# Kernel optimization log

Hardware: AMD Instinct MI355X
Metric: run time of the kernel (lower is better)

The kernel has to match this reference:

```python
import jax, jax.numpy as jnp
import numpy as np

B, H, W = 8, 256, 256
CP = 1            # pattern channels
CIN = CP + 2      # total state channels
K = 3             # neighborhood size
HID = 256         # hidden dim
ALPHA = 0.5
T_STEPS = 128
IN_DIM = CIN * K * K  # 27


def _patches(x):
    # Equivalent of tf.image.extract_patches with SAME zero padding.
    # x: [B,H,W,C] -> [B,H,W,K*K*C], ordered (kh, kw, c) with c fastest,
    # matching TF's patch flattening.
    p = (K - 1) // 2
    xp = jnp.pad(x, ((0, 0), (p, p), (p, p), (0, 0)))
    shifts = [xp[:, i:i + H, j:j + W, :] for i in range(K) for j in range(K)]
    return jnp.concatenate(shifts, axis=-1)


def setup_inputs() -> dict:
    key = jax.random.key(0)
    ks = jax.random.split(key, 5)
    state = jax.random.uniform(ks[0], (B, H, W, CIN), dtype=jnp.float32)
    # Dense layer params (glorot-ish scaling)
    W1 = jax.random.normal(ks[1], (IN_DIM, HID), dtype=jnp.float32) / np.sqrt(IN_DIM)
    b1 = jnp.zeros((HID,), dtype=jnp.float32)
    W2 = jax.random.normal(ks[2], (HID, CP), dtype=jnp.float32) / np.sqrt(HID)
    b2 = jnp.zeros((CP,), dtype=jnp.float32)
    return {"state": state, "W1": W1, "b1": b1, "W2": W2, "b2": b2}


def reference(state, W1, b1, W2, b2):
    def step(s, _):
        flat = _patches(s)                       # [B,H,W,27]
        h = jnp.tanh(flat @ W1 + b1)             # [B,H,W,HID]
        delta = h @ W2 + b2                      # [B,H,W,CP]
        pat = jnp.clip(s[..., :CP] + ALPHA * delta, 0.0, 1.0)
        s = jnp.concatenate([pat, s[..., CP:]], axis=-1)
        return s, None

    out, _ = jax.lax.scan(step, state, None, length=T_STEPS)
    return out
```

## Files before the change

kernel.cpp:

```cpp
#include <hip/hip_runtime.h>


#define BATCH 8
#define HGT 256
#define WID 256
#define NHID 256
#define ALPHA 0.5f

#define WS_W1T_OFF (BATCH * HGT * WID * 3)
#define WS_W2_OFF  (WS_W1T_OFF + 28 * NHID)

__device__ __forceinline__ float tanh_xla(float x) {
    const float cl = 7.90531110763549805f;
    float xc = fminf(fmaxf(x, -cl), cl);
    float x2 = xc * xc;
    float p = fmaf(x2, -2.76076847742355e-16f, 2.00018790482477e-13f);
    p = fmaf(x2, p, -8.60467152213735e-11f);
    p = fmaf(x2, p, 5.12229709037114e-08f);
    p = fmaf(x2, p, 1.48572235717979e-05f);
    p = fmaf(x2, p, 6.37261928875436e-04f);
    p = fmaf(x2, p, 4.89352455891786e-03f);
    p = xc * p;
    float q = fmaf(x2, 1.19825839466702e-06f, 1.18534705686654e-04f);
    q = fmaf(x2, q, 2.26843463243900e-03f);
    q = fmaf(x2, q, 4.89352518554385e-03f);
    float r = p / q;
    return (fabsf(x) < 0.0004f) ? x : r;
}

__global__ __launch_bounds__(256) void nca_prep(const float* __restrict__ W1,
                                                const float* __restrict__ b1,
                                                const float* __restrict__ W2,
                                                float* __restrict__ ws) {
    int n = threadIdx.x;
    float* w1t = ws + WS_W1T_OFF;
#pragma unroll
    for (int k = 0; k < 27; ++k) w1t[n * 28 + k] = W1[k * NHID + n];
    w1t[n * 28 + 27] = b1[n];
    ws[WS_W2_OFF + n] = W2[n];
}

#define MM1_CHAIN(P, ACC)                                   \
    do {                                                    \
        ACC = fmaf(X[0][0 + P][0], w0.x, ACC);              \
        ACC = fmaf(X[0][0 + P][1], w0.y, ACC);              \
        ACC = fmaf(X[0][0 + P][2], w0.z, ACC);              \
        ACC = fmaf(X[0][1 + P][0], w0.w, ACC);              \
        ACC = fmaf(X[0][1 + P][1], w1.x, ACC);              \
        ACC = fmaf(X[0][1 + P][2], w1.y, ACC);              \
        ACC = fmaf(X[0][2 + P][0], w1.z, ACC);              \
        ACC = fmaf(X[0][2 + P][1], w1.w, ACC);              \
        ACC = fmaf(X[0][2 + P][2], w2v.x, ACC);             \
        ACC = fmaf(X[1][0 + P][0], w2v.y, ACC);             \
        ACC = fmaf(X[1][0 + P][1], w2v.z, ACC);             \
        ACC = fmaf(X[1][0 + P][2], w2v.w, ACC);             \
        ACC = fmaf(X[1][1 + P][0], w3.x, ACC);              \
        ACC = fmaf(X[1][1 + P][1], w3.y, ACC);              \
        ACC = fmaf(X[1][1 + P][2], w3.z, ACC);              \
        ACC = fmaf(X[1][2 + P][0], w3.w, ACC);              \
        ACC = fmaf(X[1][2 + P][1], w4.x, ACC);              \
        ACC = fmaf(X[1][2 + P][2], w4.y, ACC);              \
        ACC = fmaf(X[2][0 + P][0], w4.z, ACC);              \
        ACC = fmaf(X[2][0 + P][1], w4.w, ACC);              \
        ACC = fmaf(X[2][0 + P][2], w5.x, ACC);              \
        ACC = fmaf(X[2][1 + P][0], w5.y, ACC);              \
        ACC = fmaf(X[2][1 + P][1], w5.z, ACC);              \
        ACC = fmaf(X[2][1 + P][2], w5.w, ACC);              \
        ACC = fmaf(X[2][2 + P][0], w6.x, ACC);              \
        ACC = fmaf(X[2][2 + P][1], w6.y, ACC);              \
        ACC = fmaf(X[2][2 + P][2], w6.z, ACC);              \
        ACC = ACC + w6.w;                      \
    } while (0)

__global__ __launch_bounds__(256)
__attribute__((amdgpu_waves_per_eu(2, 2)))
void nca_step(const float* __restrict__ sin,
              float* __restrict__ sout,
              const float* __restrict__ w1t,
              const float* __restrict__ w2,
              const float* __restrict__ b2p) {
    const int gid = blockIdx.x * 256 + threadIdx.x;
    const int xq = gid & 63;
    const int y  = (gid >> 6) & 255;
    const int b  = gid >> 14;
    const int x0 = xq * 4;

    float X[3][6][3];
#pragma unroll
    for (int r = 0; r < 3; ++r) {
        const int yy = y + r - 1;
        const bool yok = (yy >= 0) && (yy < HGT);
        const float* rowp = sin + (((long)b * HGT + (yok ? yy : 0)) * WID) * 3;
#pragma unroll
        for (int cc = 0; cc < 6; ++cc) {
            const int xx = x0 + cc - 1;
            const bool ok = yok && (xx >= 0) && (xx < WID);
            if (ok) {
                X[r][cc][0] = rowp[xx * 3 + 0];
                X[r][cc][1] = rowp[xx * 3 + 1];
                X[r][cc][2] = rowp[xx * 3 + 2];
            } else {
                X[r][cc][0] = 0.f; X[r][cc][1] = 0.f; X[r][cc][2] = 0.f;
            }
        }
    }
#pragma unroll
    for (int r = 0; r < 3; ++r)
#pragma unroll
        for (int cc = 0; cc < 6; ++cc)
#pragma unroll
            for (int c = 0; c < 3; ++c)
                asm volatile("" : "+v"(X[r][cc][c]));

    const float4* __restrict__ wq = (const float4*)w1t;

    float delta0 = 0.f, delta1 = 0.f, delta2 = 0.f, delta3 = 0.f;

    for (int n = 0; n < NHID; ++n) {
        const float4 w0  = wq[n * 7 + 0];
        const float4 w1  = wq[n * 7 + 1];
        const float4 w2v = wq[n * 7 + 2];
        const float4 w3  = wq[n * 7 + 3];
        const float4 w4  = wq[n * 7 + 4];
        const float4 w5  = wq[n * 7 + 5];
        const float4 w6  = wq[n * 7 + 6];
        const float  w2n = w2[n];

        float a0 = 0.f, a1 = 0.f, a2 = 0.f, a3 = 0.f;
        MM1_CHAIN(0, a0);
        MM1_CHAIN(1, a1);
        MM1_CHAIN(2, a2);
        MM1_CHAIN(3, a3);
        const float h0 = tanh_xla(a0);
        const float h1 = tanh_xla(a1);
        const float h2 = tanh_xla(a2);
        const float h3 = tanh_xla(a3);
        delta0 = fmaf(h0, w2n, delta0);
        delta1 = fmaf(h1, w2n, delta1);
        delta2 = fmaf(h2, w2n, delta2);
        delta3 = fmaf(h3, w2n, delta3);
    }

    const float b2v = b2p[0];
    float* op = sout + (((long)b * HGT + y) * WID + x0) * 3;
    float dl[4] = {delta0, delta1, delta2, delta3};
#pragma unroll
    for (int p = 0; p < 4; ++p) {
        const float s0 = X[1][p + 1][0];
        const float d  = dl[p] + b2v;
        const float td = ALPHA * d;
        float pat = s0 + td;
        pat = fminf(fmaxf(pat, 0.f), 1.f);
        op[p * 3 + 0] = pat;
        op[p * 3 + 1] = X[1][p + 1][1];
        op[p * 3 + 2] = X[1][p + 1][2];
    }
}

extern "C" void kernel_launch(void* const* d_in, const int* in_sizes, int n_in,
                              void* d_out, int out_size, void* d_ws, size_t ws_size,
                              hipStream_t stream) {
    const float* state = (const float*)d_in[0];
    const float* W1    = (const float*)d_in[1];
    const float* b1    = (const float*)d_in[2];
    const float* W2    = (const float*)d_in[3];
    const float* b2    = (const float*)d_in[4];

    float* ws_state = (float*)d_ws;
    float* w1t      = ws_state + WS_W1T_OFF;
    float* w2c      = ws_state + WS_W2_OFF;
    float* out      = (float*)d_out;

    nca_prep<<<1, 256, 0, stream>>>(W1, b1, W2, ws_state);

    const int nblocks = (BATCH * HGT * (WID / 4)) / 256;

    for (int t = 0; t < 128; ++t) {
        const float* in  = (t == 0) ? state : (((t - 1) & 1) ? out : ws_state);
        float*       dst = (t & 1) ? out : ws_state;
        nca_step<<<nblocks, 256, 0, stream>>>(in, dst, w1t, w2c, b2);
    }
}
```

Before: 19.75 ms.

## Skip MLP for pixels whose pattern neighborhood is unchanged since previous step

The pattern channel is stored as its own planar array and rotated through three buffers. The constant channels are read directly from the input state. Each thread now handles 2 pixels instead of 4, and occupancy is raised from 2 to 4 waves per EU. Each thread compares its 3x3 pattern neighborhood with the previous step's; if it is bitwise identical, the output must also be identical, so the thread copies the current value and skips the 256-wide MLP. The skip only pays off when every lane in a wavefront is at a fixed point, and the extra compare loads plus the smaller per-thread tile add cost when few pixels have settled.

```diff
diff --git a/kernel.cpp b/kernel.cpp
--- a/kernel.cpp
+++ b/kernel.cpp
@@ -5,10 +5,14 @@
 #define HGT 256
 #define WID 256
 #define NHID 256
+#define NPIX (BATCH * HGT * WID)
 #define ALPHA 0.5f
 
-#define WS_W1T_OFF (BATCH * HGT * WID * 3)
-#define WS_W2_OFF  (WS_W1T_OFF + 28 * NHID)
+#define WS_P0  0
+#define WS_P1  NPIX
+#define WS_P2  (2 * NPIX)
+#define WS_W1T (3 * NPIX)
+#define WS_W2  (WS_W1T + 28 * NHID)
 
 __device__ __forceinline__ float tanh_xla(float x) {
     const float cl = 7.90531110763549805f;
@@ -33,11 +37,28 @@
                                                 const float* __restrict__ W2,
                                                 float* __restrict__ ws) {
     int n = threadIdx.x;
-    float* w1t = ws + WS_W1T_OFF;
+    float* w1t = ws + WS_W1T;
 #pragma unroll
     for (int k = 0; k < 27; ++k) w1t[n * 28 + k] = W1[k * NHID + n];
     w1t[n * 28 + 27] = b1[n];
-    ws[WS_W2_OFF + n] = W2[n];
+    ws[WS_W2 + n] = W2[n];
+}
+
+__global__ __launch_bounds__(256) void nca_init(const float* __restrict__ state,
+                                                float* __restrict__ P0) {
+    int i = blockIdx.x * 256 + threadIdx.x;
+    if (i < NPIX) P0[i] = state[i * 3];
+}
+
+__global__ __launch_bounds__(256) void nca_final(const float* __restrict__ P,
+                                                 const float* __restrict__ cstate,
+                                                 float* __restrict__ out) {
+    int i = blockIdx.x * 256 + threadIdx.x;
+    if (i < NPIX) {
+        out[i * 3]     = P[i];
+        out[i * 3 + 1] = cstate[i * 3 + 1];
+        out[i * 3 + 2] = cstate[i * 3 + 2];
+    }
 }
 
 #define MM1_CHAIN(P, ACC)                                   \
@@ -73,48 +94,85 @@
     } while (0)
 
 __global__ __launch_bounds__(256)
-__attribute__((amdgpu_waves_per_eu(2, 2)))
-void nca_step(const float* __restrict__ sin,
-              float* __restrict__ sout,
+__attribute__((amdgpu_waves_per_eu(4, 4)))
+void nca_step(const float* __restrict__ Pprev,
+              const float* __restrict__ Pcur,
+              float* __restrict__ Pnext,
+              const float* __restrict__ cstate,
               const float* __restrict__ w1t,
               const float* __restrict__ w2,
-              const float* __restrict__ b2p) {
+              const float* __restrict__ b2p,
+              int first) {
     const int gid = blockIdx.x * 256 + threadIdx.x;
-    const int xq = gid & 63;
-    const int y  = (gid >> 6) & 255;
-    const int b  = gid >> 14;
-    const int x0 = xq * 4;
-
-    float X[3][6][3];
+    const int xq = gid & 127;
+    const int y  = (gid >> 7) & 255;
+    const int b  = gid >> 15;
+    const int x0 = xq * 2;
+
+    float Pc[3][4];
 #pragma unroll
     for (int r = 0; r < 3; ++r) {
         const int yy = y + r - 1;
         const bool yok = (yy >= 0) && (yy < HGT);
-        const float* rowp = sin + (((long)b * HGT + (yok ? yy : 0)) * WID) * 3;
-#pragma unroll
-        for (int cc = 0; cc < 6; ++cc) {
+        const float* prow = Pcur + ((long)b * HGT + (yok ? yy : 0)) * WID;
+#pragma unroll
+        for (int cc = 0; cc < 4; ++cc) {
             const int xx = x0 + cc - 1;
             const bool ok = yok && (xx >= 0) && (xx < WID);
-            if (ok) {
-                X[r][cc][0] = rowp[xx * 3 + 0];
-                X[r][cc][1] = rowp[xx * 3 + 1];
-                X[r][cc][2] = rowp[xx * 3 + 2];
-            } else {
-                X[r][cc][0] = 0.f; X[r][cc][1] = 0.f; X[r][cc][2] = 0.f;
+            Pc[r][cc] = ok ? prow[xx] : 0.f;
+        }
+    }
+
+    const long base = ((long)b * HGT + y) * WID + x0;
+
+    if (!first) {
+        bool same = true;
+#pragma unroll
+        for (int r = 0; r < 3; ++r) {
+            const int yy = y + r - 1;
+            const bool yok = (yy >= 0) && (yy < HGT);
+            const float* prow = Pprev + ((long)b * HGT + (yok ? yy : 0)) * WID;
+#pragma unroll
+            for (int cc = 0; cc < 4; ++cc) {
+                const int xx = x0 + cc - 1;
+                const bool ok = yok && (xx >= 0) && (xx < WID);
+                const float pv = ok ? prow[xx] : 0.f;
+                same = same && (__float_as_uint(Pc[r][cc]) == __float_as_uint(pv));
             }
         }
+        if (same) {
+            Pnext[base]     = Pc[1][1];
+            Pnext[base + 1] = Pc[1][2];
+            return;
+        }
+    }
+
+    float X[3][4][3];
+#pragma unroll
+    for (int r = 0; r < 3; ++r) {
+        const int yy = y + r - 1;
+        const bool yok = (yy >= 0) && (yy < HGT);
+        const float* crow = cstate + (((long)b * HGT + (yok ? yy : 0)) * WID) * 3;
+#pragma unroll
+        for (int cc = 0; cc < 4; ++cc) {
+            const int xx = x0 + cc - 1;
+            const bool ok = yok && (xx >= 0) && (xx < WID);
+            X[r][cc][0] = Pc[r][cc];
+            X[r][cc][1] = ok ? crow[xx * 3 + 1] : 0.f;
+            X[r][cc][2] = ok ? crow[xx * 3 + 2] : 0.f;
+        }
     }
 #pragma unroll
     for (int r = 0; r < 3; ++r)
 #pragma unroll
-        for (int cc = 0; cc < 6; ++cc)
+        for (int cc = 0; cc < 4; ++cc)
 #pragma unroll
             for (int c = 0; c < 3; ++c)
                 asm volatile("" : "+v"(X[r][cc][c]));
 
     const float4* __restrict__ wq = (const float4*)w1t;
 
-    float delta0 = 0.f, delta1 = 0.f, delta2 = 0.f, delta3 = 0.f;
+    float delta0 = 0.f, delta1 = 0.f;
 
     for (int n = 0; n < NHID; ++n) {
         const float4 w0  = wq[n * 7 + 0];
@@ -126,34 +184,31 @@
         const float4 w6  = wq[n * 7 + 6];
         const float  w2n = w2[n];
 
-        float a0 = 0.f, a1 = 0.f, a2 = 0.f, a3 = 0.f;
+        float a0 = 0.f, a1 = 0.f;
         MM1_CHAIN(0, a0);
         MM1_CHAIN(1, a1);
-        MM1_CHAIN(2, a2);
-        MM1_CHAIN(3, a3);
         const float h0 = tanh_xla(a0);
         const float h1 = tanh_xla(a1);
-        const float h2 = tanh_xla(a2);
-        const float h3 = tanh_xla(a3);
         delta0 = fmaf(h0, w2n, delta0);
         delta1 = fmaf(h1, w2n, delta1);
-        delta2 = fmaf(h2, w2n, delta2);
-        delta3 = fmaf(h3, w2n, delta3);
     }
 
     const float b2v = b2p[0];
-    float* op = sout + (((long)b * HGT + y) * WID + x0) * 3;
-    float dl[4] = {delta0, delta1, delta2, delta3};
-#pragma unroll
-    for (int p = 0; p < 4; ++p) {
-        const float s0 = X[1][p + 1][0];
-        const float d  = dl[p] + b2v;
+    {
+        const float s0 = Pc[1][1];
+        const float d  = delta0 + b2v;
         const float td = ALPHA * d;
         float pat = s0 + td;
         pat = fminf(fmaxf(pat, 0.f), 1.f);
-        op[p * 3 + 0] = pat;
-        op[p * 3 + 1] = X[1][p + 1][1];
-        op[p * 3 + 2] = X[1][p + 1][2];
+        Pnext[base] = pat;
+    }
+    {
+        const float s0 = Pc[1][2];
+        const float d  = delta1 + b2v;
+        const float td = ALPHA * d;
+        float pat = s0 + td;
+        pat = fminf(fmaxf(pat, 0.f), 1.f);
+        Pnext[base + 1] = pat;
     }
 }
 
@@ -166,18 +221,23 @@
     const float* W2    = (const float*)d_in[3];
     const float* b2    = (const float*)d_in[4];
 
-    float* ws_state = (float*)d_ws;
-    float* w1t      = ws_state + WS_W1T_OFF;
-    float* w2c      = ws_state + WS_W2_OFF;
-    float* out      = (float*)d_out;
-
-    nca_prep<<<1, 256, 0, stream>>>(W1, b1, W2, ws_state);
-
-    const int nblocks = (BATCH * HGT * (WID / 4)) / 256;
+    float* ws  = (float*)d_ws;
+    float* P[3] = {ws + WS_P0, ws + WS_P1, ws + WS_P2};
+    float* w1t = ws + WS_W1T;
+    float* w2c = ws + WS_W2;
+    float* out = (float*)d_out;
+
+    nca_prep<<<1, 256, 0, stream>>>(W1, b1, W2, ws);
+    nca_init<<<NPIX / 256, 256, 0, stream>>>(state, P[0]);
+
+    const int nblocks = (NPIX / 2) / 256;
 
     for (int t = 0; t < 128; ++t) {
-        const float* in  = (t == 0) ? state : (((t - 1) & 1) ? out : ws_state);
-        float*       dst = (t & 1) ? out : ws_state;
-        nca_step<<<nblocks, 256, 0, stream>>>(in, dst, w1t, w2c, b2);
-    }
-}
+        float* prv = P[(t + 2) % 3];
+        float* cur = P[t % 3];
+        float* nxt = P[(t + 1) % 3];
+        nca_step<<<nblocks, 256, 0, stream>>>(prv, cur, nxt, state,
+                                              w1t, w2c, b2, (t == 0) ? 1 : 0);
+    }
+    nca_final<<<NPIX / 256, 256, 0, stream>>>(P[128 % 3], state, out);
+}
```

Result: no change. 19.90 ms (+0.8%).

## Process two pixels per thread and force weight loads onto vector path

Applied to the files above, without the earlier changes.

Each thread now computes 2 output pixels instead of 4, doubling the grid and raising the occupancy target from 2 to 4 waves per EU. An opaque zero VGPR offset is added to the weight pointer so the compiler emits per-lane vector loads instead of scalar loads, and the hidden loop is unrolled by 2. The aim is more latency hiding through higher occupancy. The cost is less reuse of each weight load across pixels and more redundant neighbourhood loads per output.

```diff
diff --git a/kernel.cpp b/kernel.cpp
--- a/kernel.cpp
+++ b/kernel.cpp
@@ -73,26 +73,26 @@
     } while (0)
 
 __global__ __launch_bounds__(256)
-__attribute__((amdgpu_waves_per_eu(2, 2)))
+__attribute__((amdgpu_waves_per_eu(4, 4)))
 void nca_step(const float* __restrict__ sin,
               float* __restrict__ sout,
               const float* __restrict__ w1t,
               const float* __restrict__ w2,
               const float* __restrict__ b2p) {
     const int gid = blockIdx.x * 256 + threadIdx.x;
-    const int xq = gid & 63;
-    const int y  = (gid >> 6) & 255;
-    const int b  = gid >> 14;
-    const int x0 = xq * 4;
+    const int xq = gid & 127;
+    const int y  = (gid >> 7) & 255;
+    const int b  = gid >> 15;
+    const int x0 = xq * 2;
 
-    float X[3][6][3];
+    float X[3][4][3];
 #pragma unroll
     for (int r = 0; r < 3; ++r) {
         const int yy = y + r - 1;
         const bool yok = (yy >= 0) && (yy < HGT);
         const float* rowp = sin + (((long)b * HGT + (yok ? yy : 0)) * WID) * 3;
 #pragma unroll
-        for (int cc = 0; cc < 6; ++cc) {
+        for (int cc = 0; cc < 4; ++cc) {
             const int xx = x0 + cc - 1;
             const bool ok = yok && (xx >= 0) && (xx < WID);
             if (ok) {
@@ -107,53 +107,59 @@
 #pragma unroll
     for (int r = 0; r < 3; ++r)
 #pragma unroll
-        for (int cc = 0; cc < 6; ++cc)
+        for (int cc = 0; cc < 4; ++cc)
 #pragma unroll
             for (int c = 0; c < 3; ++c)
                 asm volatile("" : "+v"(X[r][cc][c]));
 
-    const float4* __restrict__ wq = (const float4*)w1t;
+    unsigned vz;
+    asm volatile("v_mov_b32 %0, 0" : "=v"(vz));
+    const float4* __restrict__ wqv =
+        (const float4*)((const char*)w1t + vz);
 
-    float delta0 = 0.f, delta1 = 0.f, delta2 = 0.f, delta3 = 0.f;
+    float delta0 = 0.f, delta1 = 0.f;
 
+#pragma unroll 2
     for (int n = 0; n < NHID; ++n) {
-        const float4 w0  = wq[n * 7 + 0];
-        const float4 w1  = wq[n * 7 + 1];
-        const float4 w2v = wq[n * 7 + 2];
-        const float4 w3  = wq[n * 7 + 3];
-        const float4 w4  = wq[n * 7 + 4];
-        const float4 w5  = wq[n * 7 + 5];
-        const float4 w6  = wq[n * 7 + 6];
+        const float4 w0  = wqv[n * 7 + 0];
+        const float4 w1  = wqv[n * 7 + 1];
+        const float4 w2v = wqv[n * 7 + 2];
+        const float4 w3  = wqv[n * 7 + 3];
+        const float4 w4  = wqv[n * 7 + 4];
+        const float4 w5  = wqv[n * 7 + 5];
+        const float4 w6  = wqv[n * 7 + 6];
         const float  w2n = w2[n];
 
-        float a0 = 0.f, a1 = 0.f, a2 = 0.f, a3 = 0.f;
+        float a0 = 0.f, a1 = 0.f;
         MM1_CHAIN(0, a0);
         MM1_CHAIN(1, a1);
-        MM1_CHAIN(2, a2);
-        MM1_CHAIN(3, a3);
         const float h0 = tanh_xla(a0);
         const float h1 = tanh_xla(a1);
-        const float h2 = tanh_xla(a2);
-        const float h3 = tanh_xla(a3);
         delta0 = fmaf(h0, w2n, delta0);
         delta1 = fmaf(h1, w2n, delta1);
-        delta2 = fmaf(h2, w2n, delta2);
-        delta3 = fmaf(h3, w2n, delta3);
     }
 
     const float b2v = b2p[0];
     float* op = sout + (((long)b * HGT + y) * WID + x0) * 3;
-    float dl[4] = {delta0, delta1, delta2, delta3};
-#pragma unroll
-    for (int p = 0; p < 4; ++p) {
-        const float s0 = X[1][p + 1][0];
-        const float d  = dl[p] + b2v;
+    {
+        const float s0 = X[1][1][0];
+        const float d  = delta0 + b2v;
         const float td = ALPHA * d;
         float pat = s0 + td;
         pat = fminf(fmaxf(pat, 0.f), 1.f);
-        op[p * 3 + 0] = pat;
-        op[p * 3 + 1] = X[1][p + 1][1];
-        op[p * 3 + 2] = X[1][p + 1][2];
+        op[0] = pat;
+        op[1] = X[1][1][1];
+        op[2] = X[1][1][2];
+    }
+    {
+        const float s0 = X[1][2][0];
+        const float d  = delta1 + b2v;
+        const float td = ALPHA * d;
+        float pat = s0 + td;
+        pat = fminf(fmaxf(pat, 0.f), 1.f);
+        op[3] = pat;
+        op[4] = X[1][2][1];
+        op[5] = X[1][2][2];
     }
 }
 
@@ -173,7 +179,7 @@
 
     nca_prep<<<1, 256, 0, stream>>>(W1, b1, W2, ws_state);
 
-    const int nblocks = (BATCH * HGT * (WID / 4)) / 256;
+    const int nblocks = (BATCH * HGT * (WID / 2)) / 256;
 
     for (int t = 0; t < 128; ++t) {
         const float* in  = (t == 0) ? state : (((t - 1) & 1) ? out : ws_state);
```

Measured after the change: 28.18 ms. 1.43x slower.
